# Kernel tuning notes

Hardware: AMD Instinct MI355X
Metric: run time of the kernel (lower is better)

## Reference

```python
import jax, jax.numpy as jnp
import numpy as np

E = 16          # num experts
D_IN = 1024     # input_size
D_OUT = 4096    # output_size
TOKENS_PER_EXPERT = 2048
TOTAL_TOKENS = E * TOKENS_PER_EXPERT


def setup_inputs() -> dict:
    key = jax.random.key(0)
    k1, k2 = jax.random.split(key)
    inputs = jax.random.normal(k1, (TOTAL_TOKENS, D_IN), dtype=jnp.float32)
    # init matches nn.init.uniform_(-1/input_size, 1/input_size)
    weight = jax.random.uniform(k2, (E, D_IN, D_OUT), dtype=jnp.float32,
                                minval=-1.0 / D_IN, maxval=1.0 / D_IN)
    # per-expert token counts; host-side numpy constant (like expert_size.tolist() in torch)
    expert_size = np.full((E,), TOKENS_PER_EXPERT, dtype=np.int64)
    return {"inputs": inputs, "expert_size": expert_size, "weight": weight}


def grouped_mm(inputs, weight, sizes):
    # sizes: python ints (static). Each contiguous chunk of tokens hits its expert's weight.
    offs = np.concatenate([[0], np.cumsum(sizes)])
    outs = [inputs[offs[i]:offs[i + 1]] @ weight[i] for i in range(len(sizes))]
    return jnp.concatenate(outs, axis=0)  # [total_tokens, D_OUT]


def reference(inputs, expert_size, weight):
    sizes = np.asarray(expert_size).tolist()  # static split sizes, as in torch.split
    return grouped_mm(inputs, weight, sizes)
```

## Files before the change

### kernel.cpp

```cpp
#include <hip/hip_runtime.h>
#include <hip/hip_bf16.h>


#define E_NUM 16
#define M_PER_E 2048
#define K_DIM 1024
#define N_DIM 4096

#define A_ELEMS (E_NUM * M_PER_E * K_DIM)
#define W_ELEMS (E_NUM * K_DIM * N_DIM)
#define WS_NEEDED ((size_t)A_ELEMS * 2 + (size_t)W_ELEMS * 2)

typedef float  float4v  __attribute__((ext_vector_type(4)));
typedef float  f32x4    __attribute__((ext_vector_type(4)));
typedef short  bf16x8   __attribute__((ext_vector_type(8)));
typedef unsigned short ushort4v __attribute__((ext_vector_type(4)));
typedef unsigned short ushort8v __attribute__((ext_vector_type(8)));

__device__ __forceinline__ ushort4v cvt4_bf16(float4v f) {
    union { __bf16 h[4]; ushort4v u; } x;
#pragma unroll
    for (int j = 0; j < 4; ++j) x.h[j] = (__bf16)f[j];
    return x.u;
}

__global__ __launch_bounds__(256) void convertA_kernel(
    const float* __restrict__ A, unsigned short* __restrict__ out, int n8)
{
    int idx = blockIdx.x * 256 + threadIdx.x;
    int stride = gridDim.x * 256;
    for (int i = idx; i < n8; i += stride) {
        float4v a = *reinterpret_cast<const float4v*>(A + (size_t)i * 8);
        float4v b = *reinterpret_cast<const float4v*>(A + (size_t)i * 8 + 4);
        ushort8v v;
        ushort4v va = cvt4_bf16(a), vb = cvt4_bf16(b);
#pragma unroll
        for (int j = 0; j < 4; ++j) { v[j] = va[j]; v[j + 4] = vb[j]; }
        *reinterpret_cast<ushort8v*>(out + (size_t)i * 8) = v;
    }
}

__global__ __launch_bounds__(256) void transposeW_kernel(
    const float* __restrict__ W, unsigned short* __restrict__ WT)
{
    const int nt = blockIdx.x;
    const int kt = blockIdx.y;
    const int e  = blockIdx.z;
    const int t  = threadIdx.x;

    __shared__ __align__(16) float T[64 * 64];

    const float* Wb = W + ((size_t)e * K_DIM + (size_t)kt * 64) * N_DIM + nt * 64;

#pragma unroll
    for (int j = 0; j < 4; ++j) {
        int kl = (t >> 4) + j * 16;
        int n4 = t & 15;
        float4v v = *reinterpret_cast<const float4v*>(Wb + (size_t)kl * N_DIM + n4 * 4);
        int sp = n4 ^ ((kl >> 3) & 7);
        *reinterpret_cast<float4v*>(&T[kl * 64 + sp * 4]) = v;
    }
    __syncthreads();

#pragma unroll
    for (int c = 0; c < 2; ++c) {
        int nl = (t >> 3) + c * 32;
        int kc = t & 7;
        ushort8v v;
#pragma unroll
        for (int j = 0; j < 8; ++j) {
            int kl = kc * 8 + j;
            int sp = (nl >> 2) ^ kc;
            float f = T[kl * 64 + sp * 4 + (nl & 3)];
            union { __bf16 h; unsigned short u; } cv; cv.h = (__bf16)f;
            v[j] = cv.u;
        }
        unsigned short* dst = WT + ((size_t)e * N_DIM + (size_t)nt * 64 + nl) * K_DIM
                              + (size_t)kt * 64 + kc * 8;
        *reinterpret_cast<ushort8v*>(dst) = v;
    }
}

#define GBM 256
#define GBN 256
#define GBK 64
#define GKT (K_DIM / GBK)

__global__ __launch_bounds__(512, 2) void gemm_bf16_kernel(
    const unsigned short* __restrict__ A,
    const unsigned short* __restrict__ B,
    float* __restrict__ C)
{
    const int bid = blockIdx.x;
    const int swzid = (bid & 7) * (2048 / 8) + (bid >> 3);
    const int e   = swzid >> 7;
    const int rem = swzid & 127;
    const int bm  = rem >> 4;
    const int bn  = rem & 15;

    const int tid  = threadIdx.x;
    const int lane = tid & 63;
    const int wid  = tid >> 6;
    const int wm   = wid >> 2;
    const int wn   = wid & 3;
    const int lrow = lane & 15;
    const int kq   = lane >> 4;

    __shared__ __align__(16) unsigned short sA[2][GBM * GBK];
    __shared__ __align__(16) unsigned short sB[2][GBN * GBK];

    const unsigned short* Abase = A + ((size_t)e * M_PER_E + (size_t)bm * GBM) * K_DIM;
    const unsigned short* Bbase = B + ((size_t)e * N_DIM  + (size_t)bn * GBN) * K_DIM;
    float*                Cbase = C + ((size_t)e * M_PER_E + (size_t)bm * GBM) * N_DIM
                                    + (size_t)bn * GBN;

    const int schunk = (lane & 7) ^ ((lane >> 3) & 7);
    const int srow   = lane >> 3;

    auto STAGE = [&](int p, int kt) {
        const unsigned short* ak = Abase + (size_t)kt * GBK + schunk * 8;
        const unsigned short* bk = Bbase + (size_t)kt * GBK + schunk * 8;
#pragma unroll
        for (int i = 0; i < 4; ++i) {
            const int rb = i * 64 + wid * 8;
            __builtin_amdgcn_global_load_lds(
                (const __attribute__((address_space(1))) void*)(ak + (size_t)(rb + srow) * K_DIM),
                (__attribute__((address_space(3))) void*)&sA[p][rb * GBK], 16, 0, 0);
            __builtin_amdgcn_global_load_lds(
                (const __attribute__((address_space(1))) void*)(bk + (size_t)(rb + srow) * K_DIM),
                (__attribute__((address_space(3))) void*)&sB[p][rb * GBK], 16, 0, 0);
        }
    };

    f32x4 acc[8][4];
#pragma unroll
    for (int mf = 0; mf < 8; ++mf)
#pragma unroll
        for (int nf = 0; nf < 4; ++nf) acc[mf][nf] = (f32x4)0.0f;

    bf16x8 af[8], bf[4];

    auto READ = [&](int p, int s) {
        const int slot = (s * 4 + kq) ^ (lrow & 7);
#pragma unroll
        for (int mf = 0; mf < 8; ++mf) {
            int row = wm * 128 + mf * 16 + lrow;
            af[mf] = *reinterpret_cast<const bf16x8*>(&sA[p][row * GBK + slot * 8]);
        }
#pragma unroll
        for (int nf = 0; nf < 4; ++nf) {
            int row = wn * 64 + nf * 16 + lrow;
            bf[nf] = *reinterpret_cast<const bf16x8*>(&sB[p][row * GBK + slot * 8]);
        }
    };

    auto MM = [&]() {
        __builtin_amdgcn_s_setprio(1);
#pragma unroll
        for (int nf = 0; nf < 4; ++nf)
#pragma unroll
            for (int mf = 0; mf < 8; ++mf)
                acc[mf][nf] = __builtin_amdgcn_mfma_f32_16x16x32_bf16(
                    af[mf], bf[nf], acc[mf][nf], 0, 0, 0);
        __builtin_amdgcn_s_setprio(0);
    };

    STAGE(0, 0);
    STAGE(1, 1);
    asm volatile("s_waitcnt vmcnt(8)" ::: "memory");
    __builtin_amdgcn_s_barrier();

#pragma unroll 1
    for (int t = 0; t < GKT; ++t) {
        const int p = t & 1;
        READ(p, 0);
        MM();
        READ(p, 1);
        asm volatile("s_waitcnt lgkmcnt(0)" ::: "memory");
        __builtin_amdgcn_s_barrier();
        if (t < GKT - 2) STAGE(p, t + 2);
        MM();
        if (t < GKT - 1) {
            if (t < GKT - 2)
                asm volatile("s_waitcnt vmcnt(8)" ::: "memory");
            else
                asm volatile("s_waitcnt vmcnt(0)" ::: "memory");
            __builtin_amdgcn_s_barrier();
        }
    }

#pragma unroll
    for (int mf = 0; mf < 8; ++mf) {
#pragma unroll
        for (int nf = 0; nf < 4; ++nf) {
#pragma unroll
            for (int j = 0; j < 4; ++j) {
                int row = wm * 128 + mf * 16 + kq * 4 + j;
                int col = wn * 64 + nf * 16 + lrow;
                Cbase[(size_t)row * N_DIM + col] = acc[mf][nf][j];
            }
        }
    }
}

#define BM 128
#define BN 128
#define BK 64
#define KT (K_DIM / BK)

__device__ __forceinline__ int swz_f(int row, int kelem) {
    return kelem ^ (((row ^ (row >> 3)) & 7) << 3);
}

__global__ __launch_bounds__(256) void grouped_gemm_fused_kernel(
    const float* __restrict__ A, const float* __restrict__ W, float* __restrict__ C)
{
    const int bn = blockIdx.x;
    const int bm = blockIdx.y;
    const int e  = blockIdx.z;
    const int tid  = threadIdx.x;
    const int lane = tid & 63;
    const int wid  = tid >> 6;
    const int wr   = wid >> 1;
    const int wc   = wid & 1;

    __shared__ __align__(16) unsigned short fA[BM * BK];
    __shared__ __align__(16) unsigned short fB[BN * BK];

    const float* Abase = A + ((size_t)e * M_PER_E + (size_t)bm * BM) * K_DIM;
    const float* Wbase = W + (size_t)e * K_DIM * N_DIM + (size_t)bn * BN;
    float*       Cbase = C + ((size_t)e * M_PER_E + (size_t)bm * BM) * N_DIM + (size_t)bn * BN;

    const int arow  = tid >> 4;
    const int acol4 = (tid & 15) * 4;
    const int bkq   = tid >> 4;
    const int bnq   = tid & 15;

    f32x4 acc[4][4];
#pragma unroll
    for (int m = 0; m < 4; ++m)
#pragma unroll
        for (int n = 0; n < 4; ++n) acc[m][n] = (f32x4)0.0f;

    float4v ra[8], rb[8];

    auto LOADT = [&](int kt) {
        const float* ap = Abase + (size_t)arow * K_DIM + kt * BK + acol4;
#pragma unroll
        for (int i = 0; i < 8; ++i)
            ra[i] = *reinterpret_cast<const float4v*>(ap + (size_t)i * 16 * K_DIM);
        const float* bp = Wbase + (size_t)(kt * BK + bkq * 4) * N_DIM + bnq * 4;
#pragma unroll
        for (int i = 0; i < 2; ++i)
#pragma unroll
            for (int r = 0; r < 4; ++r)
                rb[i * 4 + r] = *reinterpret_cast<const float4v*>(bp + (size_t)r * N_DIM + i * 64);
    };

    auto STORET = [&]() {
#pragma unroll
        for (int i = 0; i < 8; ++i) {
            int row = arow + i * 16;
            ushort4v v = cvt4_bf16(ra[i]);
            *reinterpret_cast<ushort4v*>(&fA[row * BK + swz_f(row, acol4)]) = v;
        }
#pragma unroll
        for (int i = 0; i < 2; ++i) {
#pragma unroll
            for (int j = 0; j < 4; ++j) {
                int n = (bnq + i * 16) * 4 + j;
                float4v col;
                col[0] = rb[i * 4 + 0][j];
                col[1] = rb[i * 4 + 1][j];
                col[2] = rb[i * 4 + 2][j];
                col[3] = rb[i * 4 + 3][j];
                ushort4v v = cvt4_bf16(col);
                *reinterpret_cast<ushort4v*>(&fB[n * BK + swz_f(n, bkq * 4)]) = v;
            }
        }
    };

    auto COMPUTE = [&]() {
#pragma unroll
        for (int s = 0; s < 2; ++s) {
            bf16x8 af[4], bfr[4];
            const int ke = s * 32 + (lane >> 4) * 8;
#pragma unroll
            for (int m = 0; m < 4; ++m) {
                int row = wr * 64 + m * 16 + (lane & 15);
                af[m] = *reinterpret_cast<const bf16x8*>(&fA[row * BK + swz_f(row, ke)]);
            }
#pragma unroll
            for (int n = 0; n < 4; ++n) {
                int row = wc * 64 + n * 16 + (lane & 15);
                bfr[n] = *reinterpret_cast<const bf16x8*>(&fB[row * BK + swz_f(row, ke)]);
            }
#pragma unroll
            for (int m = 0; m < 4; ++m)
#pragma unroll
                for (int n = 0; n < 4; ++n)
                    acc[m][n] = __builtin_amdgcn_mfma_f32_16x16x32_bf16(
                        af[m], bfr[n], acc[m][n], 0, 0, 0);
        }
    };

    LOADT(0);
    STORET();
    __syncthreads();
    for (int kt = 0; kt < KT; ++kt) {
        if (kt + 1 < KT) LOADT(kt + 1);
        COMPUTE();
        __syncthreads();
        if (kt + 1 < KT) STORET();
        __syncthreads();
    }

#pragma unroll
    for (int m = 0; m < 4; ++m)
#pragma unroll
        for (int n = 0; n < 4; ++n)
#pragma unroll
            for (int j = 0; j < 4; ++j) {
                int row = wr * 64 + m * 16 + (lane >> 4) * 4 + j;
                int col = wc * 64 + n * 16 + (lane & 15);
                Cbase[(size_t)row * N_DIM + col] = acc[m][n][j];
            }
}

extern "C" void kernel_launch(void* const* d_in, const int* in_sizes, int n_in,
                              void* d_out, int out_size, void* d_ws, size_t ws_size,
                              hipStream_t stream) {
    const float* A = (const float*)d_in[0];
    const float* W = (const float*)d_in[2];
    float* out = (float*)d_out;

    if (ws_size >= WS_NEEDED) {
        unsigned short* wsA = (unsigned short*)d_ws;
        unsigned short* wsW = wsA + (size_t)A_ELEMS;

        hipLaunchKernelGGL(convertA_kernel, dim3(2048), dim3(256), 0, stream,
                           A, wsA, A_ELEMS / 8);
        hipLaunchKernelGGL(transposeW_kernel, dim3(N_DIM / 64, K_DIM / 64, E_NUM),
                           dim3(256), 0, stream, W, wsW);
        hipLaunchKernelGGL(gemm_bf16_kernel, dim3(2048), dim3(512), 0, stream,
                           wsA, wsW, out);
    } else {
        dim3 grid(N_DIM / BN, M_PER_E / BM, E_NUM);
        hipLaunchKernelGGL(grouped_gemm_fused_kernel, grid, dim3(256), 0, stream,
                           A, W, out);
    }
}
```

Measured before the change: 474.6 us.

## Persistent GEMM with fine-grained quarter-tile pipeline and merged prepass kernel

Merges the A conversion and W transpose kernels into one launch. Converts the bf16 GEMM into a persistent kernel of 256 blocks, each processing 8 output tiles and prefetching the next tile's K-slices across tile boundaries. The main loop is split into quarter-tile MFMA phases with interleaved LDS reads, partial global-to-LDS staging, explicit waitcnt and sched barriers, so that loads overlap compute and the per-tile prologue and epilogue bubbles go away. It adds many barriers and intricate counter accounting, which risks stalls or errors if a waitcnt is off, and the epilogue stores are still not overlapped with compute.

Result: slower. 1.268 ms (+167.2%).

```diff
diff --git a/kernel.cpp b/kernel.cpp
--- a/kernel.cpp
+++ b/kernel.cpp
@@ -24,67 +24,72 @@
     return x.u;
 }
 
-__global__ __launch_bounds__(256) void convertA_kernel(
-    const float* __restrict__ A, unsigned short* __restrict__ out, int n8)
+__global__ __launch_bounds__(256) void prepass_kernel(
+    const float* __restrict__ A, const float* __restrict__ W,
+    unsigned short* __restrict__ outA, unsigned short* __restrict__ outW)
 {
-    int idx = blockIdx.x * 256 + threadIdx.x;
-    int stride = gridDim.x * 256;
-    for (int i = idx; i < n8; i += stride) {
-        float4v a = *reinterpret_cast<const float4v*>(A + (size_t)i * 8);
-        float4v b = *reinterpret_cast<const float4v*>(A + (size_t)i * 8 + 4);
-        ushort8v v;
-        ushort4v va = cvt4_bf16(a), vb = cvt4_bf16(b);
-#pragma unroll
-        for (int j = 0; j < 4; ++j) { v[j] = va[j]; v[j + 4] = vb[j]; }
-        *reinterpret_cast<ushort8v*>(out + (size_t)i * 8) = v;
-    }
-}
-
-__global__ __launch_bounds__(256) void transposeW_kernel(
-    const float* __restrict__ W, unsigned short* __restrict__ WT)
-{
-    const int nt = blockIdx.x;
-    const int kt = blockIdx.y;
-    const int e  = blockIdx.z;
-    const int t  = threadIdx.x;
-
     __shared__ __align__(16) float T[64 * 64];
-
-    const float* Wb = W + ((size_t)e * K_DIM + (size_t)kt * 64) * N_DIM + nt * 64;
-
-#pragma unroll
-    for (int j = 0; j < 4; ++j) {
-        int kl = (t >> 4) + j * 16;
-        int n4 = t & 15;
-        float4v v = *reinterpret_cast<const float4v*>(Wb + (size_t)kl * N_DIM + n4 * 4);
-        int sp = n4 ^ ((kl >> 3) & 7);
-        *reinterpret_cast<float4v*>(&T[kl * 64 + sp * 4]) = v;
-    }
-    __syncthreads();
-
-#pragma unroll
-    for (int c = 0; c < 2; ++c) {
-        int nl = (t >> 3) + c * 32;
-        int kc = t & 7;
-        ushort8v v;
-#pragma unroll
-        for (int j = 0; j < 8; ++j) {
-            int kl = kc * 8 + j;
-            int sp = (nl >> 2) ^ kc;
-            float f = T[kl * 64 + sp * 4 + (nl & 3)];
-            union { __bf16 h; unsigned short u; } cv; cv.h = (__bf16)f;
-            v[j] = cv.u;
-        }
-        unsigned short* dst = WT + ((size_t)e * N_DIM + (size_t)nt * 64 + nl) * K_DIM
-                              + (size_t)kt * 64 + kc * 8;
-        *reinterpret_cast<ushort8v*>(dst) = v;
+    const int b = blockIdx.x;
+    const int t = threadIdx.x;
+
+    if (b < 16384) {
+        const int nt = b & 63;
+        const int kt = (b >> 6) & 15;
+        const int e  = b >> 10;
+        const float* Wb = W + ((size_t)e * K_DIM + (size_t)kt * 64) * N_DIM + nt * 64;
+
+#pragma unroll
+        for (int j = 0; j < 4; ++j) {
+            int kl = (t >> 4) + j * 16;
+            int n4 = t & 15;
+            float4v v = *reinterpret_cast<const float4v*>(Wb + (size_t)kl * N_DIM + n4 * 4);
+            int sp = n4 ^ ((kl >> 3) & 7);
+            *reinterpret_cast<float4v*>(&T[kl * 64 + sp * 4]) = v;
+        }
+        __syncthreads();
+
+#pragma unroll
+        for (int c = 0; c < 2; ++c) {
+            int nl = (t >> 3) + c * 32;
+            int kc = t & 7;
+            ushort8v v;
+#pragma unroll
+            for (int j = 0; j < 8; ++j) {
+                int kl = kc * 8 + j;
+                int sp = (nl >> 2) ^ kc;
+                float f = T[kl * 64 + sp * 4 + (nl & 3)];
+                union { __bf16 h; unsigned short u; } cv; cv.h = (__bf16)f;
+                v[j] = cv.u;
+            }
+            unsigned short* dst = outW + ((size_t)e * N_DIM + (size_t)nt * 64 + nl) * K_DIM
+                                  + (size_t)kt * 64 + kc * 8;
+            *reinterpret_cast<ushort8v*>(dst) = v;
+        }
+    } else {
+        const int n8 = A_ELEMS / 8;
+        int idx = (b - 16384) * 256 + t;
+        int stride = 2048 * 256;
+        for (int i = idx; i < n8; i += stride) {
+            float4v a = *reinterpret_cast<const float4v*>(A + (size_t)i * 8);
+            float4v bb = *reinterpret_cast<const float4v*>(A + (size_t)i * 8 + 4);
+            ushort8v v;
+            ushort4v va = cvt4_bf16(a), vb = cvt4_bf16(bb);
+#pragma unroll
+            for (int j = 0; j < 4; ++j) { v[j] = va[j]; v[j + 4] = vb[j]; }
+            *reinterpret_cast<ushort8v*>(outA + (size_t)i * 8) = v;
+        }
     }
 }
 
 #define GBM 256
 #define GBN 256
 #define GBK 64
-#define GKT (K_DIM / GBK)
+#define NT_TOTAL 128
+
+#define BARX()  __builtin_amdgcn_s_barrier()
+#define SB0()   __builtin_amdgcn_sched_barrier(0)
+#define LGKM(N) asm volatile("s_waitcnt lgkmcnt(" #N ")" ::: "memory")
+#define VMC(N)  asm volatile("s_waitcnt vmcnt(" #N ")" ::: "memory")
 
 __global__ __launch_bounds__(512, 2) void gemm_bf16_kernel(
     const unsigned short* __restrict__ A,
@@ -92,11 +97,8 @@
     float* __restrict__ C)
 {
     const int bid = blockIdx.x;
-    const int swzid = (bid & 7) * (2048 / 8) + (bid >> 3);
-    const int e   = swzid >> 7;
-    const int rem = swzid & 127;
-    const int bm  = rem >> 4;
-    const int bn  = rem & 15;
+    const int x   = bid & 7;
+    const int sl  = bid >> 3;
 
     const int tid  = threadIdx.x;
     const int lane = tid & 63;
@@ -109,26 +111,47 @@
     __shared__ __align__(16) unsigned short sA[2][GBM * GBK];
     __shared__ __align__(16) unsigned short sB[2][GBN * GBK];
 
-    const unsigned short* Abase = A + ((size_t)e * M_PER_E + (size_t)bm * GBM) * K_DIM;
-    const unsigned short* Bbase = B + ((size_t)e * N_DIM  + (size_t)bn * GBN) * K_DIM;
-    float*                Cbase = C + ((size_t)e * M_PER_E + (size_t)bm * GBM) * N_DIM
-                                    + (size_t)bn * GBN;
-
     const int schunk = (lane & 7) ^ ((lane >> 3) & 7);
     const int srow   = lane >> 3;
 
-    auto STAGE = [&](int p, int kt) {
-        const unsigned short* ak = Abase + (size_t)kt * GBK + schunk * 8;
-        const unsigned short* bk = Bbase + (size_t)kt * GBK + schunk * 8;
-#pragma unroll
-        for (int i = 0; i < 4; ++i) {
-            const int rb = i * 64 + wid * 8;
+    const unsigned short *Acur, *Bcur, *Anext, *Bnext;
+    float* Ccur;
+    int jj = 0;
+
+    auto setBasesAB = [&](int j, const unsigned short*& Ab, const unsigned short*& Bb) {
+        int swz = x * 256 + j * 32 + sl;
+        int e = swz >> 7, rem = swz & 127, bm = rem >> 4, bn = rem & 15;
+        Ab = A + ((size_t)e * M_PER_E + (size_t)bm * GBM) * K_DIM;
+        Bb = B + ((size_t)e * N_DIM  + (size_t)bn * GBN) * K_DIM;
+    };
+    auto setBaseC = [&](int j) {
+        int swz = x * 256 + j * 32 + sl;
+        int e = swz >> 7, rem = swz & 127, bm = rem >> 4, bn = rem & 15;
+        Ccur = C + ((size_t)e * M_PER_E + (size_t)bm * GBM) * N_DIM + (size_t)bn * GBN;
+    };
+
+    auto STAGE_AQ = [&](int g, int q) {
+        if (g >= NT_TOTAL) return;
+        const unsigned short* base = ((g >> 4) == jj) ? Acur : Anext;
+        const unsigned short* src = base + (size_t)(q * 64 + wid * 8 + srow) * K_DIM
+                                    + (g & 15) * GBK + schunk * 8;
+        __builtin_amdgcn_global_load_lds(
+            (const __attribute__((address_space(1))) void*)src,
+            (__attribute__((address_space(3))) void*)&sA[g & 1][(q * 64 + wid * 8) * GBK],
+            16, 0, 0);
+    };
+    auto STAGE_BH = [&](int g, int h) {
+        if (g >= NT_TOTAL) return;
+        const unsigned short* base = ((g >> 4) == jj) ? Bcur : Bnext;
+#pragma unroll
+        for (int j2 = 0; j2 < 2; ++j2) {
+            int rb = h * 128 + (wid * 2 + j2) * 8;
+            const unsigned short* src = base + (size_t)(rb + srow) * K_DIM
+                                        + (g & 15) * GBK + schunk * 8;
             __builtin_amdgcn_global_load_lds(
-                (const __attribute__((address_space(1))) void*)(ak + (size_t)(rb + srow) * K_DIM),
-                (__attribute__((address_space(3))) void*)&sA[p][rb * GBK], 16, 0, 0);
-            __builtin_amdgcn_global_load_lds(
-                (const __attribute__((address_space(1))) void*)(bk + (size_t)(rb + srow) * K_DIM),
-                (__attribute__((address_space(3))) void*)&sB[p][rb * GBK], 16, 0, 0);
+                (const __attribute__((address_space(1))) void*)src,
+                (__attribute__((address_space(3))) void*)&sB[g & 1][rb * GBK],
+                16, 0, 0);
         }
     };
 
@@ -138,66 +161,117 @@
 #pragma unroll
         for (int nf = 0; nf < 4; ++nf) acc[mf][nf] = (f32x4)0.0f;
 
-    bf16x8 af[8], bf[4];
-
-    auto READ = [&](int p, int s) {
+    bf16x8 afP[4], afQ[4], bfP[4], bfQ[4];
+
+    auto READ_AF = [&](bf16x8* dst, int p, int mh, int s) {
         const int slot = (s * 4 + kq) ^ (lrow & 7);
 #pragma unroll
-        for (int mf = 0; mf < 8; ++mf) {
-            int row = wm * 128 + mf * 16 + lrow;
-            af[mf] = *reinterpret_cast<const bf16x8*>(&sA[p][row * GBK + slot * 8]);
-        }
+        for (int mf = 0; mf < 4; ++mf) {
+            int row = wm * 128 + mh * 64 + mf * 16 + lrow;
+            dst[mf] = *reinterpret_cast<const bf16x8*>(&sA[p][row * GBK + slot * 8]);
+        }
+    };
+    auto READ_BF = [&](bf16x8* dst, int p, int s) {
+        const int slot = (s * 4 + kq) ^ (lrow & 7);
 #pragma unroll
         for (int nf = 0; nf < 4; ++nf) {
             int row = wn * 64 + nf * 16 + lrow;
-            bf[nf] = *reinterpret_cast<const bf16x8*>(&sB[p][row * GBK + slot * 8]);
-        }
-    };
-
-    auto MM = [&]() {
+            dst[nf] = *reinterpret_cast<const bf16x8*>(&sB[p][row * GBK + slot * 8]);
+        }
+    };
+    auto MMQ = [&](const bf16x8* af, const bf16x8* bf, int mh) {
         __builtin_amdgcn_s_setprio(1);
 #pragma unroll
         for (int nf = 0; nf < 4; ++nf)
 #pragma unroll
-            for (int mf = 0; mf < 8; ++mf)
-                acc[mf][nf] = __builtin_amdgcn_mfma_f32_16x16x32_bf16(
-                    af[mf], bf[nf], acc[mf][nf], 0, 0, 0);
+            for (int mf = 0; mf < 4; ++mf)
+                acc[mh * 4 + mf][nf] = __builtin_amdgcn_mfma_f32_16x16x32_bf16(
+                    af[mf], bf[nf], acc[mh * 4 + mf][nf], 0, 0, 0);
         __builtin_amdgcn_s_setprio(0);
     };
 
-    STAGE(0, 0);
-    STAGE(1, 1);
-    asm volatile("s_waitcnt vmcnt(8)" ::: "memory");
-    __builtin_amdgcn_s_barrier();
+    setBasesAB(0, Acur, Bcur);
+    setBasesAB(1, Anext, Bnext);
+    setBaseC(0);
+    STAGE_AQ(0, 0); STAGE_AQ(0, 1); STAGE_AQ(0, 2); STAGE_AQ(0, 3);
+    STAGE_BH(0, 0); STAGE_BH(0, 1);
+    STAGE_BH(1, 0); STAGE_BH(1, 1);
+    VMC(4);
+    BARX();
+    READ_AF(afP, 0, 0, 0);
+    READ_BF(bfP, 0, 0);
 
 #pragma unroll 1
-    for (int t = 0; t < GKT; ++t) {
-        const int p = t & 1;
-        READ(p, 0);
-        MM();
-        READ(p, 1);
-        asm volatile("s_waitcnt lgkmcnt(0)" ::: "memory");
-        __builtin_amdgcn_s_barrier();
-        if (t < GKT - 2) STAGE(p, t + 2);
-        MM();
-        if (t < GKT - 1) {
-            if (t < GKT - 2)
-                asm volatile("s_waitcnt vmcnt(8)" ::: "memory");
-            else
-                asm volatile("s_waitcnt vmcnt(0)" ::: "memory");
-            __builtin_amdgcn_s_barrier();
-        }
-    }
-
-#pragma unroll
-    for (int mf = 0; mf < 8; ++mf) {
-#pragma unroll
-        for (int nf = 0; nf < 4; ++nf) {
-#pragma unroll
-            for (int j = 0; j < 4; ++j) {
-                int row = wm * 128 + mf * 16 + kq * 4 + j;
-                int col = wn * 64 + nf * 16 + lrow;
-                Cbase[(size_t)row * N_DIM + col] = acc[mf][nf][j];
+    for (jj = 0; jj < 8; ++jj) {
+        if (jj) {
+            setBasesAB(jj, Acur, Bcur);
+            int jn = (jj < 7) ? jj + 1 : 7;
+            setBasesAB(jn, Anext, Bnext);
+            setBaseC(jj);
+        }
+#pragma unroll 1
+        for (int i = 0; i < 8; ++i) {
+            const int g = jj * 16 + 2 * i;
+            READ_AF(afQ, 0, 1, 0);
+            STAGE_AQ(g + 1, 0); STAGE_AQ(g + 1, 2);
+            BARX(); LGKM(4); SB0();
+            MMQ(afP, bfP, 0);
+            BARX();
+            READ_AF(afP, 0, 0, 1); READ_BF(bfQ, 0, 1);
+            STAGE_AQ(g + 1, 1); STAGE_AQ(g + 1, 3);
+            BARX(); LGKM(8); SB0();
+            MMQ(afQ, bfP, 1);
+            BARX();
+            READ_AF(afQ, 0, 1, 1);
+            BARX(); LGKM(4); SB0();
+            MMQ(afP, bfQ, 0);
+            VMC(2);
+            BARX();
+            READ_AF(afP, 1, 0, 0); READ_BF(bfP, 1, 0);
+            STAGE_BH(g + 2, 0);
+            BARX(); LGKM(8); SB0();
+            MMQ(afQ, bfQ, 1);
+            VMC(2);
+            BARX();
+            READ_AF(afQ, 1, 1, 0);
+            STAGE_BH(g + 2, 1);
+            BARX(); LGKM(4); SB0();
+            MMQ(afP, bfP, 0);
+            BARX();
+            READ_AF(afP, 1, 0, 1); READ_BF(bfQ, 1, 1);
+            STAGE_AQ(g + 2, 0); STAGE_AQ(g + 2, 2);
+            BARX(); LGKM(8); SB0();
+            MMQ(afQ, bfP, 1);
+            BARX();
+            READ_AF(afQ, 1, 1, 1);
+            STAGE_AQ(g + 2, 1); STAGE_AQ(g + 2, 3);
+            BARX(); LGKM(4); SB0();
+            MMQ(afP, bfQ, 0);
+            VMC(2);
+            BARX();
+            if (g + 2 < NT_TOTAL) {
+                READ_AF(afP, 0, 0, 0); READ_BF(bfP, 0, 0);
+            }
+            STAGE_BH(g + 3, 0); STAGE_BH(g + 3, 1);
+            BARX();
+            if (g + 2 < NT_TOTAL) { LGKM(8); } else { LGKM(0); }
+            SB0();
+            MMQ(afQ, bfQ, 1);
+            VMC(4);
+            BARX();
+        }
+
+#pragma unroll
+        for (int mf = 0; mf < 8; ++mf) {
+#pragma unroll
+            for (int nf = 0; nf < 4; ++nf) {
+#pragma unroll
+                for (int j = 0; j < 4; ++j) {
+                    int row = wm * 128 + mf * 16 + kq * 4 + j;
+                    int col = wn * 64 + nf * 16 + lrow;
+                    Ccur[(size_t)row * N_DIM + col] = acc[mf][nf][j];
+                }
+                acc[mf][nf] = (f32x4)0.0f;
             }
         }
     }
@@ -338,11 +412,9 @@
         unsigned short* wsA = (unsigned short*)d_ws;
         unsigned short* wsW = wsA + (size_t)A_ELEMS;
 
-        hipLaunchKernelGGL(convertA_kernel, dim3(2048), dim3(256), 0, stream,
-                           A, wsA, A_ELEMS / 8);
-        hipLaunchKernelGGL(transposeW_kernel, dim3(N_DIM / 64, K_DIM / 64, E_NUM),
-                           dim3(256), 0, stream, W, wsW);
-        hipLaunchKernelGGL(gemm_bf16_kernel, dim3(2048), dim3(512), 0, stream,
+        hipLaunchKernelGGL(prepass_kernel, dim3(18432), dim3(256), 0, stream,
+                           A, W, wsA, wsW);
+        hipLaunchKernelGGL(gemm_bf16_kernel, dim3(256), dim3(512), 0, stream,
                            wsA, wsW, out);
     } else {
         dim3 grid(N_DIM / BN, M_PER_E / BM, E_NUM);
```
